# Kernel tuning notes

Hardware: AMD Instinct MI355X
Metric: run time of the kernel (lower is better)

Reference implementation:

```python
import jax, jax.numpy as jnp
import numpy as np

B, N, C = 2, 2048, 1024
H = 16
HD = C // H  # 64


def setup_inputs() -> dict:
    key = jax.random.key(0)
    k1, k2, k3 = jax.random.split(key, 3)
    x = jax.random.normal(k1, (B, N, C), dtype=jnp.float32)
    w_qkv = jax.random.normal(k2, (C, 3 * C), dtype=jnp.float32) * (C ** -0.5)
    b_qkv = jnp.zeros((3 * C,), dtype=jnp.float32)
    w_out = jax.random.normal(k3, (C, C), dtype=jnp.float32) * (C ** -0.5)
    b_out = jnp.zeros((C,), dtype=jnp.float32)
    return {"x": x, "w_qkv": w_qkv, "b_qkv": b_qkv, "w_out": w_out, "b_out": b_out}


def reference(x, w_qkv, b_qkv, w_out, b_out):
    scale = HD ** -0.5
    # QKV projection: (B,N,3C) -> (B,N,3,H,HD) -> (B,3,H,N,HD)
    qkv = (jnp.einsum('bnc,cd->bnd', x, w_qkv) + b_qkv)
    qkv = qkv.reshape(B, N, 3, H, HD).transpose(0, 2, 3, 1, 4)
    q, k, v = qkv[:, 0], qkv[:, 1], qkv[:, 2]  # each (B,H,N,HD)
    # scaled dot-product attention with full NxN matrix (as in source)
    attn = jnp.einsum('bhnd,bhmd->bhnm', q, k) * scale
    attn = jax.nn.softmax(attn, axis=-1)
    out = jnp.einsum('bhnm,bhmd->bhnd', attn, v)  # (B,H,N,HD)
    out = out.transpose(0, 2, 1, 3).reshape(B, N, C)
    out = jnp.einsum('bnc,cd->bnd', out, w_out) + b_out
    return out
```

## Files before the change

### kernel.cpp

```cpp
#include <hip/hip_runtime.h>
#include <stdint.h>

using uint = unsigned int;
using ushort = unsigned short;

constexpr int Bb = 2;
constexpr int Ns = 2048;
constexpr int Cd = 1024;
constexpr int Hh = 16;
constexpr int HD = 64;
constexpr int BHND = Bb * Hh * Ns * HD;

constexpr float QSCL = 0.18033688f;

typedef __attribute__((ext_vector_type(8))) short short8;
typedef __attribute__((ext_vector_type(4))) float floatx4;

__device__ inline ushort f2bf(float f) {
  uint u = __float_as_uint(f);
  return (ushort)((u + 0x7fffu + ((u >> 16) & 1u)) >> 16);
}
__device__ inline ushort f2bfr(float f) {
  return (ushort)((__float_as_uint(f) + 0x8000u) >> 16);
}
__device__ inline uint cvt_pk_bf16(float lo, float hi) {
  uint r;
  asm("v_cvt_pk_bf16_f32 %0, %1, %2" : "=v"(r) : "v"(lo), "v"(hi));
  return r;
}
__device__ inline void gld_lds16(const ushort* g, ushort* l) {
  __builtin_amdgcn_global_load_lds(
      (const __attribute__((address_space(1))) uint*)g,
      (__attribute__((address_space(3))) uint*)l, 16, 0, 0);
}

__global__ __launch_bounds__(256) void cvt_f32_bf16(
    const float* __restrict__ in, ushort* __restrict__ outp) {
  const int i = blockIdx.x * 256 + threadIdx.x;
  const float4 v = ((const float4*)in)[i];
  ushort4 o;
  o.x = f2bf(v.x); o.y = f2bf(v.y); o.z = f2bf(v.z); o.w = f2bf(v.w);
  ((ushort4*)outp)[i] = o;
}

__global__ __launch_bounds__(256) void transpose_f32_bf16(
    const float* __restrict__ in, ushort* __restrict__ outp, int R, int Cc) {
  __shared__ alignas(16) ushort tile[32][33];
  const int c0 = blockIdx.x * 32, r0 = blockIdx.y * 32;
  const int tx = threadIdx.x & 31;
  const int ty = threadIdx.x >> 5;
#pragma unroll
  for (int i = 0; i < 4; ++i)
    tile[ty + 8 * i][tx] = f2bf(in[(size_t)(r0 + ty + 8 * i) * Cc + c0 + tx]);
  __syncthreads();
#pragma unroll
  for (int i = 0; i < 4; ++i)
    outp[(size_t)(c0 + ty + 8 * i) * R + r0 + tx] = tile[tx][ty + 8 * i];
}

__global__ __launch_bounds__(256) void gemm_qkv(
    const ushort* __restrict__ A, const ushort* __restrict__ Bt,
    const float* __restrict__ bias, ushort* __restrict__ outp,
    int M, int K, int Nn) {
  __shared__ alignas(16) ushort As[2][128 * 32];
  __shared__ alignas(16) ushort Bs[2][128 * 32];
  const int tid = threadIdx.x;
  const int wave = tid >> 6, lane = tid & 63;
  const int quad = lane >> 4, l16 = lane & 15;
  const int wr = wave >> 1, wc = wave & 1;
  const int m0 = blockIdx.x * 128, n0 = blockIdx.y * 128;

  const int lrow = lane >> 2;
  const int lgr = lane & 3;
  const ushort* pa = A + (size_t)(m0 + wave * 32 + lrow) * K + lgr * 8;
  const ushort* pb = Bt + (size_t)(n0 + wave * 32 + lrow) * K + lgr * 8;
  const int lofs = wave * 32 * 32;

  floatx4 acc[4][4];
#pragma unroll
  for (int i = 0; i < 4; ++i)
#pragma unroll
    for (int j = 0; j < 4; ++j) {
      acc[i][j][0] = 0.f; acc[i][j][1] = 0.f; acc[i][j][2] = 0.f; acc[i][j][3] = 0.f;
    }

  const int nkt = K >> 5;
  gld_lds16(pa, &As[0][lofs]);
  gld_lds16(pa + (size_t)16 * K, &As[0][lofs + 16 * 32]);
  gld_lds16(pb, &Bs[0][lofs]);
  gld_lds16(pb + (size_t)16 * K, &Bs[0][lofs + 16 * 32]);
  __syncthreads();

  int cur = 0;
  for (int kt = 0; kt < nkt; ++kt) {
    if (kt + 1 < nkt) {
      const ushort* qa = pa + (size_t)(kt + 1) * 32;
      const ushort* qb = pb + (size_t)(kt + 1) * 32;
      gld_lds16(qa, &As[cur ^ 1][lofs]);
      gld_lds16(qa + (size_t)16 * K, &As[cur ^ 1][lofs + 16 * 32]);
      gld_lds16(qb, &Bs[cur ^ 1][lofs]);
      gld_lds16(qb + (size_t)16 * K, &Bs[cur ^ 1][lofs + 16 * 32]);
    }
    short8 af[4], bfv[4];
#pragma unroll
    for (int mt = 0; mt < 4; ++mt)
      af[mt] = *(const short8*)&As[cur][(wr * 64 + mt * 16 + l16) * 32 + quad * 8];
#pragma unroll
    for (int nt = 0; nt < 4; ++nt)
      bfv[nt] = *(const short8*)&Bs[cur][(wc * 64 + nt * 16 + l16) * 32 + quad * 8];
#pragma unroll
    for (int mt = 0; mt < 4; ++mt)
#pragma unroll
      for (int nt = 0; nt < 4; ++nt)
        acc[mt][nt] = __builtin_amdgcn_mfma_f32_16x16x32_bf16(af[mt], bfv[nt],
                                                              acc[mt][nt], 0, 0, 0);
    __syncthreads();
    cur ^= 1;
  }

  ushort* qp = outp;
  ushort* kp = qp + BHND;
  ushort* vp = qp + 2 * BHND;
#pragma unroll
  for (int nt = 0; nt < 4; ++nt) {
    const int gn = n0 + wc * 64 + nt * 16 + l16;
    const float bv = bias[gn];
    const int which = gn >> 10, cc = gn & 1023;
    const int h = cc >> 6, d = cc & 63;
    const float sc = (which == 0) ? QSCL : 1.0f;
#pragma unroll
    for (int mt = 0; mt < 4; ++mt) {
#pragma unroll
      for (int r = 0; r < 4; ++r) {
        const int gm = m0 + wr * 64 + mt * 16 + quad * 4 + r;
        const int b = gm >> 11, n = gm & 2047;
        const ushort o = f2bfr((acc[mt][nt][r] + bv) * sc);
        const int bh = b * Hh + h;
        if (which == 0)
          qp[((size_t)bh * Ns + n) * HD + d] = o;
        else if (which == 1)
          kp[((size_t)bh * Ns + n) * HD + d] = o;
        else
          vp[((size_t)bh * HD + d) * Ns + n] = o;
      }
    }
  }
}

__global__ __launch_bounds__(256) void gemm_out(
    const ushort* __restrict__ A, const ushort* __restrict__ Bt,
    const float* __restrict__ bias, float* __restrict__ fout,
    int M, int K, int Nn) {
  constexpr int LDT = 40;
  __shared__ alignas(16) ushort As[128 * LDT];
  __shared__ alignas(16) ushort Bs[128 * LDT];
  const int tid = threadIdx.x;
  const int wave = tid >> 6, lane = tid & 63;
  const int quad = lane >> 4, l16 = lane & 15;
  const int wr = wave >> 1, wc = wave & 1;
  const int m0 = blockIdx.x * 128, n0 = blockIdx.y * 128;

  const int srow0 = tid >> 2;
  const int skc = (tid & 3) * 8;

  const ushort* pa = A + (size_t)(m0 + srow0) * K + skc;
  const ushort* pb = Bt + (size_t)(n0 + srow0) * K + skc;

  floatx4 acc[4][4];
#pragma unroll
  for (int i = 0; i < 4; ++i)
#pragma unroll
    for (int j = 0; j < 4; ++j) {
      acc[i][j][0] = 0.f; acc[i][j][1] = 0.f; acc[i][j][2] = 0.f; acc[i][j][3] = 0.f;
    }

  uint4 ra0 = *(const uint4*)(pa);
  uint4 ra1 = *(const uint4*)(pa + (size_t)64 * K);
  uint4 rb0 = *(const uint4*)(pb);
  uint4 rb1 = *(const uint4*)(pb + (size_t)64 * K);

  const int nkt = K >> 5;
  for (int kt = 0; kt < nkt; ++kt) {
    __syncthreads();
    *(uint4*)&As[srow0 * LDT + skc] = ra0;
    *(uint4*)&As[(srow0 + 64) * LDT + skc] = ra1;
    *(uint4*)&Bs[srow0 * LDT + skc] = rb0;
    *(uint4*)&Bs[(srow0 + 64) * LDT + skc] = rb1;
    __syncthreads();
    if (kt + 1 < nkt) {
      const ushort* qa = pa + (size_t)(kt + 1) * 32;
      const ushort* qb = pb + (size_t)(kt + 1) * 32;
      ra0 = *(const uint4*)(qa);
      ra1 = *(const uint4*)(qa + (size_t)64 * K);
      rb0 = *(const uint4*)(qb);
      rb1 = *(const uint4*)(qb + (size_t)64 * K);
    }
    short8 af[4], bfv[4];
#pragma unroll
    for (int mt = 0; mt < 4; ++mt)
      af[mt] = *(const short8*)&As[(wr * 64 + mt * 16 + l16) * LDT + quad * 8];
#pragma unroll
    for (int nt = 0; nt < 4; ++nt)
      bfv[nt] = *(const short8*)&Bs[(wc * 64 + nt * 16 + l16) * LDT + quad * 8];
#pragma unroll
    for (int mt = 0; mt < 4; ++mt)
#pragma unroll
      for (int nt = 0; nt < 4; ++nt)
        acc[mt][nt] = __builtin_amdgcn_mfma_f32_16x16x32_bf16(af[mt], bfv[nt],
                                                              acc[mt][nt], 0, 0, 0);
  }

#pragma unroll
  for (int nt = 0; nt < 4; ++nt) {
    const int gn = n0 + wc * 64 + nt * 16 + l16;
    const float bv = bias[gn];
#pragma unroll
    for (int mt = 0; mt < 4; ++mt)
#pragma unroll
      for (int r = 0; r < 4; ++r) {
        const int gm = m0 + wr * 64 + mt * 16 + quad * 4 + r;
        fout[(size_t)gm * Nn + gn] = acc[mt][nt][r] + bv;
      }
  }
}

__global__ __launch_bounds__(256, 2) void attn(
    const ushort* __restrict__ q, const ushort* __restrict__ k,
    const ushort* __restrict__ vT, ushort* __restrict__ aout) {
  constexpr int LDK = 72;
  __shared__ alignas(16) ushort Ks[64 * LDK];
  __shared__ alignas(16) ushort Vs[64 * LDK];
  const int tid = threadIdx.x;
  const int wave = tid >> 6, lane = tid & 63;
  const int quad = lane >> 4, l16 = lane & 15;
  const int bh = blockIdx.y;
  const int qw = blockIdx.x * 128 + wave * 32;

  const ushort* kb = k + (size_t)bh * Ns * HD;
  const ushort* vb = vT + (size_t)bh * HD * Ns;

  short8 aq[2][2];
#pragma unroll
  for (int nqi = 0; nqi < 2; ++nqi) {
    const ushort* qp = q + ((size_t)bh * Ns + qw + nqi * 16 + l16) * HD + quad * 8;
    aq[nqi][0] = *(const short8*)(qp);
    aq[nqi][1] = *(const short8*)(qp + 32);
  }

  floatx4 accO[4][2];
#pragma unroll
  for (int mt = 0; mt < 4; ++mt)
#pragma unroll
    for (int nqi = 0; nqi < 2; ++nqi) {
      accO[mt][nqi][0] = 0.f; accO[mt][nqi][1] = 0.f;
      accO[mt][nqi][2] = 0.f; accO[mt][nqi][3] = 0.f;
    }
  float lst[2] = {0.f, 0.f};
  const floatx4 fz = {0.f, 0.f, 0.f, 0.f};

  const int srow = tid >> 2;
  const int g0 = (tid & 3) * 2;
  const int cbA = (g0 >> 2) * 8 + ((g0 >> 1) & 1);
  const int g1 = g0 + 1;
  const int cbB = (g1 >> 2) * 8 + 4 + ((g1 >> 1) & 1);

  const ushort* kgp = kb + (size_t)srow * HD + g0 * 8;
  const ushort* vgp = vb + (size_t)srow * Ns + g0 * 8;
  ushort* ksw = &Ks[srow * LDK + g0 * 8];
  ushort* vswA = &Vs[srow * LDK + cbA * 4];
  ushort* vswB = &Vs[srow * LDK + cbB * 4];

  uint4 kg0 = *(const uint4*)(kgp);
  uint4 kg1 = *(const uint4*)(kgp + 8);
  uint4 vg0 = *(const uint4*)(vgp);
  uint4 vg1 = *(const uint4*)(vgp + 8);
  const ushort* kpre = kgp + 64 * HD;
  const ushort* vpre = vgp + 64;

  for (int kv0 = 0; kv0 < Ns; kv0 += 64) {
    __syncthreads();
    *(uint4*)ksw = kg0;
    *(uint4*)(ksw + 8) = kg1;
    *(uint2*)vswA = make_uint2(vg0.x, vg0.y);
    *(uint2*)(vswA + 8) = make_uint2(vg0.z, vg0.w);
    *(uint2*)vswB = make_uint2(vg1.x, vg1.y);
    *(uint2*)(vswB + 8) = make_uint2(vg1.z, vg1.w);
    __syncthreads();

    short8 ak[4][2], av[4][2];
#pragma unroll
    for (int t4 = 0; t4 < 4; ++t4) {
      const int ro = (t4 * 16 + l16) * LDK + quad * 8;
      ak[t4][0] = *(const short8*)&Ks[ro];
      ak[t4][1] = *(const short8*)&Ks[ro + 32];
      av[t4][0] = *(const short8*)&Vs[ro];
      av[t4][1] = *(const short8*)&Vs[ro + 32];
    }
    if (kv0 + 64 < Ns) {
      kg0 = *(const uint4*)(kpre);
      kg1 = *(const uint4*)(kpre + 8);
      vg0 = *(const uint4*)(vpre);
      vg1 = *(const uint4*)(vpre + 8);
      kpre += 64 * HD;
      vpre += 64;
    }

#pragma unroll
    for (int nqi = 0; nqi < 2; ++nqi) {
      floatx4 sacc[4];
      __builtin_amdgcn_s_setprio(1);
#pragma unroll
      for (int kvt = 0; kvt < 4; ++kvt)
        sacc[kvt] = __builtin_amdgcn_mfma_f32_16x16x32_bf16(
            ak[kvt][0], aq[nqi][0], fz, 0, 0, 0);
#pragma unroll
      for (int kvt = 0; kvt < 4; ++kvt)
        sacc[kvt] = __builtin_amdgcn_mfma_f32_16x16x32_bf16(
            ak[kvt][1], aq[nqi][1], sacc[kvt], 0, 0, 0);
      __builtin_amdgcn_s_setprio(0);

      uint pk[4][2];
      float ls = 0.f;
#pragma unroll
      for (int kvt = 0; kvt < 4; ++kvt) {
        const float p0 = __builtin_amdgcn_exp2f(sacc[kvt][0]);
        const float p1 = __builtin_amdgcn_exp2f(sacc[kvt][1]);
        const float p2 = __builtin_amdgcn_exp2f(sacc[kvt][2]);
        const float p3 = __builtin_amdgcn_exp2f(sacc[kvt][3]);
        ls += (p0 + p1) + (p2 + p3);
        pk[kvt][0] = cvt_pk_bf16(p0, p1);
        pk[kvt][1] = cvt_pk_bf16(p2, p3);
      }
      lst[nqi] += ls;

      __builtin_amdgcn_s_setprio(1);
#pragma unroll
      for (int ks = 0; ks < 2; ++ks) {
        union { uint u[4]; short8 s; } pf;
        pf.u[0] = pk[2 * ks][0]; pf.u[1] = pk[2 * ks][1];
        pf.u[2] = pk[2 * ks + 1][0]; pf.u[3] = pk[2 * ks + 1][1];
#pragma unroll
        for (int mt = 0; mt < 4; ++mt)
          accO[mt][nqi] = __builtin_amdgcn_mfma_f32_16x16x32_bf16(
              av[mt][ks], pf.s, accO[mt][nqi], 0, 0, 0);
      }
      __builtin_amdgcn_s_setprio(0);
    }
  }

  const int b = bh >> 4, h = bh & 15;
#pragma unroll
  for (int nqi = 0; nqi < 2; ++nqi) {
    float l = lst[nqi];
    l += __shfl_xor(l, 16, 64);
    l += __shfl_xor(l, 32, 64);
    const float inv = 1.f / l;
    const int n = qw + nqi * 16 + l16;
#pragma unroll
    for (int mt = 0; mt < 4; ++mt) {
      ushort4 o;
      o.x = f2bfr(accO[mt][nqi][0] * inv);
      o.y = f2bfr(accO[mt][nqi][1] * inv);
      o.z = f2bfr(accO[mt][nqi][2] * inv);
      o.w = f2bfr(accO[mt][nqi][3] * inv);
      *(ushort4*)&aout[((size_t)(b * Ns + n)) * Cd + h * HD + mt * 16 + quad * 4] = o;
    }
  }
}

extern "C" void kernel_launch(void* const* d_in, const int* in_sizes, int n_in,
                              void* d_out, int out_size, void* d_ws, size_t ws_size,
                              hipStream_t stream) {
  (void)in_sizes; (void)n_in; (void)out_size; (void)ws_size;
  const float* x = (const float*)d_in[0];
  const float* w_qkv = (const float*)d_in[1];
  const float* b_qkv = (const float*)d_in[2];
  const float* w_out = (const float*)d_in[3];
  const float* b_out = (const float*)d_in[4];

  ushort* xbf = (ushort*)d_ws;
  ushort* wqkvT = xbf + (size_t)BHND;
  ushort* woutT = wqkvT + 3072 * 1024;
  ushort* qkvbuf = woutT + 1024 * 1024;
  ushort* aout = qkvbuf + 3 * (size_t)BHND;

  cvt_f32_bf16<<<dim3(BHND / 1024), 256, 0, stream>>>(x, xbf);
  transpose_f32_bf16<<<dim3(96, 32), 256, 0, stream>>>(w_qkv, wqkvT, 1024, 3072);
  transpose_f32_bf16<<<dim3(32, 32), 256, 0, stream>>>(w_out, woutT, 1024, 1024);

  gemm_qkv<<<dim3(32, 24), 256, 0, stream>>>(xbf, wqkvT, b_qkv, qkvbuf,
                                             4096, 1024, 3072);
  attn<<<dim3(16, 32), 256, 0, stream>>>(qkvbuf, qkvbuf + BHND,
                                         qkvbuf + 2 * (size_t)BHND, aout);
  gemm_out<<<dim3(32, 8), 256, 0, stream>>>(aout, woutT, b_out, (float*)d_out,
                                            4096, 1024, 1024);
}
```

Baseline: 186.7 us.

## Merge prep kernels into one launch and double attention KV tile to 128

Fuses the x conversion and both weight transposes into a single prep kernel dispatched by block index, removing two kernel launches. In attention, each iteration now stages 128 keys/values in LDS instead of 64, halving the number of barrier pairs and issuing prefetches for a larger chunk. This costs more LDS and registers per block, which may reduce occupancy or increase spills.

New measurement: 188.9 us. About the same (+1.2%).

```diff
diff --git a/kernel.cpp b/kernel.cpp
--- a/kernel.cpp
+++ b/kernel.cpp
@@ -34,21 +34,31 @@
       (__attribute__((address_space(3))) uint*)l, 16, 0, 0);
 }
 
-__global__ __launch_bounds__(256) void cvt_f32_bf16(
-    const float* __restrict__ in, ushort* __restrict__ outp) {
-  const int i = blockIdx.x * 256 + threadIdx.x;
-  const float4 v = ((const float4*)in)[i];
-  ushort4 o;
-  o.x = f2bf(v.x); o.y = f2bf(v.y); o.z = f2bf(v.z); o.w = f2bf(v.w);
-  ((ushort4*)outp)[i] = o;
-}
-
-__global__ __launch_bounds__(256) void transpose_f32_bf16(
-    const float* __restrict__ in, ushort* __restrict__ outp, int R, int Cc) {
+__global__ __launch_bounds__(256) void prep(
+    const float* __restrict__ x, ushort* __restrict__ xbf,
+    const float* __restrict__ w_qkv, ushort* __restrict__ wqkvT,
+    const float* __restrict__ w_out, ushort* __restrict__ woutT) {
   __shared__ alignas(16) ushort tile[32][33];
-  const int c0 = blockIdx.x * 32, r0 = blockIdx.y * 32;
-  const int tx = threadIdx.x & 31;
-  const int ty = threadIdx.x >> 5;
+  const int bid = blockIdx.x;
+  const int tid = threadIdx.x;
+  if (bid < 4096) {
+    const int i = bid * 256 + tid;
+    const float4 v = ((const float4*)x)[i];
+    ushort4 o;
+    o.x = f2bf(v.x); o.y = f2bf(v.y); o.z = f2bf(v.z); o.w = f2bf(v.w);
+    ((ushort4*)xbf)[i] = o;
+    return;
+  }
+  const float* in;
+  ushort* outp;
+  int Cc, idx;
+  if (bid < 7168) { idx = bid - 4096; in = w_qkv; outp = wqkvT; Cc = 3072; }
+  else            { idx = bid - 7168; in = w_out; outp = woutT; Cc = 1024; }
+  const int R = 1024;
+  const int nbx = Cc >> 5;
+  const int bx = idx % nbx, by = idx / nbx;
+  const int c0 = bx * 32, r0 = by * 32;
+  const int tx = tid & 31, ty = tid >> 5;
 #pragma unroll
   for (int i = 0; i < 4; ++i)
     tile[ty + 8 * i][tx] = f2bf(in[(size_t)(r0 + ty + 8 * i) * Cc + c0 + tx]);
@@ -228,8 +238,9 @@
     const ushort* __restrict__ q, const ushort* __restrict__ k,
     const ushort* __restrict__ vT, ushort* __restrict__ aout) {
   constexpr int LDK = 72;
-  __shared__ alignas(16) ushort Ks[64 * LDK];
-  __shared__ alignas(16) ushort Vs[64 * LDK];
+  constexpr int LDV = 136;
+  __shared__ alignas(16) ushort Ks[128 * LDK];
+  __shared__ alignas(16) ushort Vs[64 * LDV];
   const int tid = threadIdx.x;
   const int wave = tid >> 6, lane = tid & 63;
   const int quad = lane >> 4, l16 = lane & 15;
@@ -259,92 +270,122 @@
   const floatx4 fz = {0.f, 0.f, 0.f, 0.f};
 
   const int srow = tid >> 2;
-  const int g0 = (tid & 3) * 2;
-  const int cbA = (g0 >> 2) * 8 + ((g0 >> 1) & 1);
-  const int g1 = g0 + 1;
-  const int cbB = (g1 >> 2) * 8 + 4 + ((g1 >> 1) & 1);
-
-  const ushort* kgp = kb + (size_t)srow * HD + g0 * 8;
-  const ushort* vgp = vb + (size_t)srow * Ns + g0 * 8;
-  ushort* ksw = &Ks[srow * LDK + g0 * 8];
-  ushort* vswA = &Vs[srow * LDK + cbA * 4];
-  ushort* vswB = &Vs[srow * LDK + cbB * 4];
-
-  uint4 kg0 = *(const uint4*)(kgp);
-  uint4 kg1 = *(const uint4*)(kgp + 8);
+  const int gk = (tid & 3) * 2;
+  const ushort* kgp0 = kb + (size_t)srow * HD + gk * 8;
+  const ushort* kgp1 = kb + (size_t)(srow + 64) * HD + gk * 8;
+  ushort* ksw0 = &Ks[srow * LDK + gk * 8];
+  ushort* ksw1 = &Ks[(srow + 64) * LDK + gk * 8];
+
+  const int G0 = (tid & 3) * 4;
+  const int sHalf = G0 >> 3;
+  const int gp0 = G0 & 7;
+  const int cb0 = (gp0 >> 2) * 8 + ((gp0 >> 1) & 1);
+  const int cb1 = ((gp0 + 1) >> 2) * 8 + 4 + (((gp0 + 1) >> 1) & 1);
+  const int cb2 = ((gp0 + 2) >> 2) * 8 + (((gp0 + 2) >> 1) & 1);
+  const int cb3 = ((gp0 + 3) >> 2) * 8 + 4 + (((gp0 + 3) >> 1) & 1);
+  ushort* vw0 = &Vs[srow * LDV + sHalf * 64 + cb0 * 4];
+  ushort* vw1 = &Vs[srow * LDV + sHalf * 64 + cb1 * 4];
+  ushort* vw2 = &Vs[srow * LDV + sHalf * 64 + cb2 * 4];
+  ushort* vw3 = &Vs[srow * LDV + sHalf * 64 + cb3 * 4];
+  const ushort* vgp = vb + (size_t)srow * Ns + G0 * 8;
+
+  uint4 kg0 = *(const uint4*)(kgp0);
+  uint4 kg1 = *(const uint4*)(kgp0 + 8);
+  uint4 kg2 = *(const uint4*)(kgp1);
+  uint4 kg3 = *(const uint4*)(kgp1 + 8);
   uint4 vg0 = *(const uint4*)(vgp);
   uint4 vg1 = *(const uint4*)(vgp + 8);
-  const ushort* kpre = kgp + 64 * HD;
-  const ushort* vpre = vgp + 64;
-
-  for (int kv0 = 0; kv0 < Ns; kv0 += 64) {
+  uint4 vg2 = *(const uint4*)(vgp + 16);
+  uint4 vg3 = *(const uint4*)(vgp + 24);
+  const ushort* kpre0 = kgp0 + 128 * HD;
+  const ushort* kpre1 = kgp1 + 128 * HD;
+  const ushort* vpre = vgp + 128;
+
+  for (int kv0 = 0; kv0 < Ns; kv0 += 128) {
     __syncthreads();
-    *(uint4*)ksw = kg0;
-    *(uint4*)(ksw + 8) = kg1;
-    *(uint2*)vswA = make_uint2(vg0.x, vg0.y);
-    *(uint2*)(vswA + 8) = make_uint2(vg0.z, vg0.w);
-    *(uint2*)vswB = make_uint2(vg1.x, vg1.y);
-    *(uint2*)(vswB + 8) = make_uint2(vg1.z, vg1.w);
+    *(uint4*)ksw0 = kg0;
+    *(uint4*)(ksw0 + 8) = kg1;
+    *(uint4*)ksw1 = kg2;
+    *(uint4*)(ksw1 + 8) = kg3;
+    *(uint2*)vw0 = make_uint2(vg0.x, vg0.y);
+    *(uint2*)(vw0 + 8) = make_uint2(vg0.z, vg0.w);
+    *(uint2*)vw1 = make_uint2(vg1.x, vg1.y);
+    *(uint2*)(vw1 + 8) = make_uint2(vg1.z, vg1.w);
+    *(uint2*)vw2 = make_uint2(vg2.x, vg2.y);
+    *(uint2*)(vw2 + 8) = make_uint2(vg2.z, vg2.w);
+    *(uint2*)vw3 = make_uint2(vg3.x, vg3.y);
+    *(uint2*)(vw3 + 8) = make_uint2(vg3.z, vg3.w);
     __syncthreads();
 
-    short8 ak[4][2], av[4][2];
-#pragma unroll
-    for (int t4 = 0; t4 < 4; ++t4) {
-      const int ro = (t4 * 16 + l16) * LDK + quad * 8;
-      ak[t4][0] = *(const short8*)&Ks[ro];
-      ak[t4][1] = *(const short8*)&Ks[ro + 32];
-      av[t4][0] = *(const short8*)&Vs[ro];
-      av[t4][1] = *(const short8*)&Vs[ro + 32];
-    }
-    if (kv0 + 64 < Ns) {
-      kg0 = *(const uint4*)(kpre);
-      kg1 = *(const uint4*)(kpre + 8);
-      vg0 = *(const uint4*)(vpre);
-      vg1 = *(const uint4*)(vpre + 8);
-      kpre += 64 * HD;
-      vpre += 64;
-    }
-
-#pragma unroll
-    for (int nqi = 0; nqi < 2; ++nqi) {
-      floatx4 sacc[4];
-      __builtin_amdgcn_s_setprio(1);
-#pragma unroll
-      for (int kvt = 0; kvt < 4; ++kvt)
-        sacc[kvt] = __builtin_amdgcn_mfma_f32_16x16x32_bf16(
-            ak[kvt][0], aq[nqi][0], fz, 0, 0, 0);
-#pragma unroll
-      for (int kvt = 0; kvt < 4; ++kvt)
-        sacc[kvt] = __builtin_amdgcn_mfma_f32_16x16x32_bf16(
-            ak[kvt][1], aq[nqi][1], sacc[kvt], 0, 0, 0);
-      __builtin_amdgcn_s_setprio(0);
-
-      uint pk[4][2];
-      float ls = 0.f;
-#pragma unroll
-      for (int kvt = 0; kvt < 4; ++kvt) {
-        const float p0 = __builtin_amdgcn_exp2f(sacc[kvt][0]);
-        const float p1 = __builtin_amdgcn_exp2f(sacc[kvt][1]);
-        const float p2 = __builtin_amdgcn_exp2f(sacc[kvt][2]);
-        const float p3 = __builtin_amdgcn_exp2f(sacc[kvt][3]);
-        ls += (p0 + p1) + (p2 + p3);
-        pk[kvt][0] = cvt_pk_bf16(p0, p1);
-        pk[kvt][1] = cvt_pk_bf16(p2, p3);
+    bool first = true;
+#pragma unroll
+    for (int st = 0; st < 2; ++st) {
+      short8 ak[4][2], av[4][2];
+#pragma unroll
+      for (int t4 = 0; t4 < 4; ++t4) {
+        const int rk = (st * 64 + t4 * 16 + l16) * LDK + quad * 8;
+        const int rv = (t4 * 16 + l16) * LDV + st * 64 + quad * 8;
+        ak[t4][0] = *(const short8*)&Ks[rk];
+        ak[t4][1] = *(const short8*)&Ks[rk + 32];
+        av[t4][0] = *(const short8*)&Vs[rv];
+        av[t4][1] = *(const short8*)&Vs[rv + 32];
       }
-      lst[nqi] += ls;
-
-      __builtin_amdgcn_s_setprio(1);
-#pragma unroll
-      for (int ks = 0; ks < 2; ++ks) {
-        union { uint u[4]; short8 s; } pf;
-        pf.u[0] = pk[2 * ks][0]; pf.u[1] = pk[2 * ks][1];
-        pf.u[2] = pk[2 * ks + 1][0]; pf.u[3] = pk[2 * ks + 1][1];
-#pragma unroll
-        for (int mt = 0; mt < 4; ++mt)
-          accO[mt][nqi] = __builtin_amdgcn_mfma_f32_16x16x32_bf16(
-              av[mt][ks], pf.s, accO[mt][nqi], 0, 0, 0);
+      if (first && kv0 + 128 < Ns) {
+        kg0 = *(const uint4*)(kpre0);
+        kg1 = *(const uint4*)(kpre0 + 8);
+        kg2 = *(const uint4*)(kpre1);
+        kg3 = *(const uint4*)(kpre1 + 8);
+        vg0 = *(const uint4*)(vpre);
+        vg1 = *(const uint4*)(vpre + 8);
+        vg2 = *(const uint4*)(vpre + 16);
+        vg3 = *(const uint4*)(vpre + 24);
+        kpre0 += 128 * HD;
+        kpre1 += 128 * HD;
+        vpre += 128;
       }
-      __builtin_amdgcn_s_setprio(0);
+      first = false;
+
+#pragma unroll
+      for (int nqi = 0; nqi < 2; ++nqi) {
+        floatx4 sacc[4];
+        __builtin_amdgcn_s_setprio(1);
+#pragma unroll
+        for (int kvt = 0; kvt < 4; ++kvt)
+          sacc[kvt] = __builtin_amdgcn_mfma_f32_16x16x32_bf16(
+              ak[kvt][0], aq[nqi][0], fz, 0, 0, 0);
+#pragma unroll
+        for (int kvt = 0; kvt < 4; ++kvt)
+          sacc[kvt] = __builtin_amdgcn_mfma_f32_16x16x32_bf16(
+              ak[kvt][1], aq[nqi][1], sacc[kvt], 0, 0, 0);
+        __builtin_amdgcn_s_setprio(0);
+
+        uint pk[4][2];
+        float ls = 0.f;
+#pragma unroll
+        for (int kvt = 0; kvt < 4; ++kvt) {
+          const float p0 = __builtin_amdgcn_exp2f(sacc[kvt][0]);
+          const float p1 = __builtin_amdgcn_exp2f(sacc[kvt][1]);
+          const float p2 = __builtin_amdgcn_exp2f(sacc[kvt][2]);
+          const float p3 = __builtin_amdgcn_exp2f(sacc[kvt][3]);
+          ls += (p0 + p1) + (p2 + p3);
+          pk[kvt][0] = cvt_pk_bf16(p0, p1);
+          pk[kvt][1] = cvt_pk_bf16(p2, p3);
+        }
+        lst[nqi] += ls;
+
+        __builtin_amdgcn_s_setprio(1);
+#pragma unroll
+        for (int ks = 0; ks < 2; ++ks) {
+          union { uint u[4]; short8 s; } pf;
+          pf.u[0] = pk[2 * ks][0]; pf.u[1] = pk[2 * ks][1];
+          pf.u[2] = pk[2 * ks + 1][0]; pf.u[3] = pk[2 * ks + 1][1];
+#pragma unroll
+          for (int mt = 0; mt < 4; ++mt)
+            accO[mt][nqi] = __builtin_amdgcn_mfma_f32_16x16x32_bf16(
+                av[mt][ks], pf.s, accO[mt][nqi], 0, 0, 0);
+        }
+        __builtin_amdgcn_s_setprio(0);
+      }
     }
   }
 
@@ -384,9 +425,7 @@
   ushort* qkvbuf = woutT + 1024 * 1024;
   ushort* aout = qkvbuf + 3 * (size_t)BHND;
 
-  cvt_f32_bf16<<<dim3(BHND / 1024), 256, 0, stream>>>(x, xbf);
-  transpose_f32_bf16<<<dim3(96, 32), 256, 0, stream>>>(w_qkv, wqkvT, 1024, 3072);
-  transpose_f32_bf16<<<dim3(32, 32), 256, 0, stream>>>(w_out, woutT, 1024, 1024);
+  prep<<<dim3(8192), 256, 0, stream>>>(x, xbf, w_qkv, wqkvT, w_out, woutT);
 
   gemm_qkv<<<dim3(32, 24), 256, 0, stream>>>(xbf, wqkvT, b_qkv, qkvbuf,
                                              4096, 1024, 3072);
```

## Double-buffer K/V tiles in attention and merge prep kernels into one launch

Applied to the files above, without the earlier changes.

The attention kernel now keeps two LDS buffers for K and V. The next tile's global loads are written into the alternate buffer after compute, which cuts the per-tile barriers from two to one. The three preprocessing kernels (x conversion and two weight transposes) are fused into a single launch that dispatches on block index, saving launch overhead. LDS usage doubles, which may reduce occupancy for the attention kernel.

New measurement: 183.5 us. No clear change (-1.7%).

```diff
diff --git a/kernel.cpp b/kernel.cpp
--- a/kernel.cpp
+++ b/kernel.cpp
@@ -34,21 +34,31 @@
       (__attribute__((address_space(3))) uint*)l, 16, 0, 0);
 }
 
-__global__ __launch_bounds__(256) void cvt_f32_bf16(
-    const float* __restrict__ in, ushort* __restrict__ outp) {
-  const int i = blockIdx.x * 256 + threadIdx.x;
-  const float4 v = ((const float4*)in)[i];
-  ushort4 o;
-  o.x = f2bf(v.x); o.y = f2bf(v.y); o.z = f2bf(v.z); o.w = f2bf(v.w);
-  ((ushort4*)outp)[i] = o;
-}
-
-__global__ __launch_bounds__(256) void transpose_f32_bf16(
-    const float* __restrict__ in, ushort* __restrict__ outp, int R, int Cc) {
+__global__ __launch_bounds__(256) void prep(
+    const float* __restrict__ x, ushort* __restrict__ xbf,
+    const float* __restrict__ w_qkv, ushort* __restrict__ wqkvT,
+    const float* __restrict__ w_out, ushort* __restrict__ woutT) {
   __shared__ alignas(16) ushort tile[32][33];
-  const int c0 = blockIdx.x * 32, r0 = blockIdx.y * 32;
-  const int tx = threadIdx.x & 31;
-  const int ty = threadIdx.x >> 5;
+  const int bid = blockIdx.x;
+  const int tid = threadIdx.x;
+  if (bid < 4096) {
+    const int i = bid * 256 + tid;
+    const float4 v = ((const float4*)x)[i];
+    ushort4 o;
+    o.x = f2bf(v.x); o.y = f2bf(v.y); o.z = f2bf(v.z); o.w = f2bf(v.w);
+    ((ushort4*)xbf)[i] = o;
+    return;
+  }
+  const float* in;
+  ushort* outp;
+  int Cc, idx;
+  if (bid < 7168) { idx = bid - 4096; in = w_qkv; outp = wqkvT; Cc = 3072; }
+  else            { idx = bid - 7168; in = w_out; outp = woutT; Cc = 1024; }
+  const int R = 1024;
+  const int nbx = Cc >> 5;
+  const int bx = idx % nbx, by = idx / nbx;
+  const int c0 = bx * 32, r0 = by * 32;
+  const int tx = tid & 31, ty = tid >> 5;
 #pragma unroll
   for (int i = 0; i < 4; ++i)
     tile[ty + 8 * i][tx] = f2bf(in[(size_t)(r0 + ty + 8 * i) * Cc + c0 + tx]);
@@ -228,8 +238,8 @@
     const ushort* __restrict__ q, const ushort* __restrict__ k,
     const ushort* __restrict__ vT, ushort* __restrict__ aout) {
   constexpr int LDK = 72;
-  __shared__ alignas(16) ushort Ks[64 * LDK];
-  __shared__ alignas(16) ushort Vs[64 * LDK];
+  __shared__ alignas(16) ushort Ks[2][64 * LDK];
+  __shared__ alignas(16) ushort Vs[2][64 * LDK];
   const int tid = threadIdx.x;
   const int wave = tid >> 6, lane = tid & 63;
   const int quad = lane >> 4, l16 = lane & 15;
@@ -266,9 +276,9 @@
 
   const ushort* kgp = kb + (size_t)srow * HD + g0 * 8;
   const ushort* vgp = vb + (size_t)srow * Ns + g0 * 8;
-  ushort* ksw = &Ks[srow * LDK + g0 * 8];
-  ushort* vswA = &Vs[srow * LDK + cbA * 4];
-  ushort* vswB = &Vs[srow * LDK + cbB * 4];
+  const int kofs = srow * LDK + g0 * 8;
+  const int vofsA = srow * LDK + cbA * 4;
+  const int vofsB = srow * LDK + cbB * 4;
 
   uint4 kg0 = *(const uint4*)(kgp);
   uint4 kg1 = *(const uint4*)(kgp + 8);
@@ -277,74 +287,88 @@
   const ushort* kpre = kgp + 64 * HD;
   const ushort* vpre = vgp + 64;
 
-  for (int kv0 = 0; kv0 < Ns; kv0 += 64) {
-    __syncthreads();
-    *(uint4*)ksw = kg0;
-    *(uint4*)(ksw + 8) = kg1;
-    *(uint2*)vswA = make_uint2(vg0.x, vg0.y);
-    *(uint2*)(vswA + 8) = make_uint2(vg0.z, vg0.w);
-    *(uint2*)vswB = make_uint2(vg1.x, vg1.y);
-    *(uint2*)(vswB + 8) = make_uint2(vg1.z, vg1.w);
-    __syncthreads();
-
-    short8 ak[4][2], av[4][2];
-#pragma unroll
-    for (int t4 = 0; t4 < 4; ++t4) {
-      const int ro = (t4 * 16 + l16) * LDK + quad * 8;
-      ak[t4][0] = *(const short8*)&Ks[ro];
-      ak[t4][1] = *(const short8*)&Ks[ro + 32];
-      av[t4][0] = *(const short8*)&Vs[ro];
-      av[t4][1] = *(const short8*)&Vs[ro + 32];
-    }
-    if (kv0 + 64 < Ns) {
-      kg0 = *(const uint4*)(kpre);
-      kg1 = *(const uint4*)(kpre + 8);
-      vg0 = *(const uint4*)(vpre);
-      vg1 = *(const uint4*)(vpre + 8);
-      kpre += 64 * HD;
-      vpre += 64;
-    }
-
-#pragma unroll
-    for (int nqi = 0; nqi < 2; ++nqi) {
-      floatx4 sacc[4];
-      __builtin_amdgcn_s_setprio(1);
-#pragma unroll
-      for (int kvt = 0; kvt < 4; ++kvt)
-        sacc[kvt] = __builtin_amdgcn_mfma_f32_16x16x32_bf16(
-            ak[kvt][0], aq[nqi][0], fz, 0, 0, 0);
-#pragma unroll
-      for (int kvt = 0; kvt < 4; ++kvt)
-        sacc[kvt] = __builtin_amdgcn_mfma_f32_16x16x32_bf16(
-            ak[kvt][1], aq[nqi][1], sacc[kvt], 0, 0, 0);
-      __builtin_amdgcn_s_setprio(0);
-
-      uint pk[4][2];
-      float ls = 0.f;
-#pragma unroll
-      for (int kvt = 0; kvt < 4; ++kvt) {
-        const float p0 = __builtin_amdgcn_exp2f(sacc[kvt][0]);
-        const float p1 = __builtin_amdgcn_exp2f(sacc[kvt][1]);
-        const float p2 = __builtin_amdgcn_exp2f(sacc[kvt][2]);
-        const float p3 = __builtin_amdgcn_exp2f(sacc[kvt][3]);
-        ls += (p0 + p1) + (p2 + p3);
-        pk[kvt][0] = cvt_pk_bf16(p0, p1);
-        pk[kvt][1] = cvt_pk_bf16(p2, p3);
-      }
-      lst[nqi] += ls;
-
-      __builtin_amdgcn_s_setprio(1);
-#pragma unroll
-      for (int ks = 0; ks < 2; ++ks) {
-        union { uint u[4]; short8 s; } pf;
-        pf.u[0] = pk[2 * ks][0]; pf.u[1] = pk[2 * ks][1];
-        pf.u[2] = pk[2 * ks + 1][0]; pf.u[3] = pk[2 * ks + 1][1];
-#pragma unroll
-        for (int mt = 0; mt < 4; ++mt)
-          accO[mt][nqi] = __builtin_amdgcn_mfma_f32_16x16x32_bf16(
-              av[mt][ks], pf.s, accO[mt][nqi], 0, 0, 0);
-      }
-      __builtin_amdgcn_s_setprio(0);
+  *(uint4*)&Ks[0][kofs] = kg0;
+  *(uint4*)&Ks[0][kofs + 8] = kg1;
+  *(uint2*)&Vs[0][vofsA] = make_uint2(vg0.x, vg0.y);
+  *(uint2*)&Vs[0][vofsA + 8] = make_uint2(vg0.z, vg0.w);
+  *(uint2*)&Vs[0][vofsB] = make_uint2(vg1.x, vg1.y);
+  *(uint2*)&Vs[0][vofsB + 8] = make_uint2(vg1.z, vg1.w);
+  __syncthreads();
+
+  for (int kv0 = 0; kv0 < Ns; kv0 += 128) {
+#pragma unroll
+    for (int half = 0; half < 2; ++half) {
+      const bool more = kv0 + 64 * (half + 1) < Ns;
+
+      short8 ak[4][2], av[4][2];
+#pragma unroll
+      for (int t4 = 0; t4 < 4; ++t4) {
+        const int ro = (t4 * 16 + l16) * LDK + quad * 8;
+        ak[t4][0] = *(const short8*)&Ks[half][ro];
+        ak[t4][1] = *(const short8*)&Ks[half][ro + 32];
+        av[t4][0] = *(const short8*)&Vs[half][ro];
+        av[t4][1] = *(const short8*)&Vs[half][ro + 32];
+      }
+      if (more) {
+        kg0 = *(const uint4*)(kpre);
+        kg1 = *(const uint4*)(kpre + 8);
+        vg0 = *(const uint4*)(vpre);
+        vg1 = *(const uint4*)(vpre + 8);
+        kpre += 64 * HD;
+        vpre += 64;
+      }
+
+#pragma unroll
+      for (int nqi = 0; nqi < 2; ++nqi) {
+        floatx4 sacc[4];
+        __builtin_amdgcn_s_setprio(1);
+#pragma unroll
+        for (int kvt = 0; kvt < 4; ++kvt)
+          sacc[kvt] = __builtin_amdgcn_mfma_f32_16x16x32_bf16(
+              ak[kvt][0], aq[nqi][0], fz, 0, 0, 0);
+#pragma unroll
+        for (int kvt = 0; kvt < 4; ++kvt)
+          sacc[kvt] = __builtin_amdgcn_mfma_f32_16x16x32_bf16(
+              ak[kvt][1], aq[nqi][1], sacc[kvt], 0, 0, 0);
+        __builtin_amdgcn_s_setprio(0);
+
+        uint pk[4][2];
+        float ls = 0.f;
+#pragma unroll
+        for (int kvt = 0; kvt < 4; ++kvt) {
+          const float p0 = __builtin_amdgcn_exp2f(sacc[kvt][0]);
+          const float p1 = __builtin_amdgcn_exp2f(sacc[kvt][1]);
+          const float p2 = __builtin_amdgcn_exp2f(sacc[kvt][2]);
+          const float p3 = __builtin_amdgcn_exp2f(sacc[kvt][3]);
+          ls += (p0 + p1) + (p2 + p3);
+          pk[kvt][0] = cvt_pk_bf16(p0, p1);
+          pk[kvt][1] = cvt_pk_bf16(p2, p3);
+        }
+        lst[nqi] += ls;
+
+        __builtin_amdgcn_s_setprio(1);
+#pragma unroll
+        for (int ks = 0; ks < 2; ++ks) {
+          union { uint u[4]; short8 s; } pf;
+          pf.u[0] = pk[2 * ks][0]; pf.u[1] = pk[2 * ks][1];
+          pf.u[2] = pk[2 * ks + 1][0]; pf.u[3] = pk[2 * ks + 1][1];
+#pragma unroll
+          for (int mt = 0; mt < 4; ++mt)
+            accO[mt][nqi] = __builtin_amdgcn_mfma_f32_16x16x32_bf16(
+                av[mt][ks], pf.s, accO[mt][nqi], 0, 0, 0);
+        }
+        __builtin_amdgcn_s_setprio(0);
+      }
+
+      if (more) {
+        *(uint4*)&Ks[half ^ 1][kofs] = kg0;
+        *(uint4*)&Ks[half ^ 1][kofs + 8] = kg1;
+        *(uint2*)&Vs[half ^ 1][vofsA] = make_uint2(vg0.x, vg0.y);
+        *(uint2*)&Vs[half ^ 1][vofsA + 8] = make_uint2(vg0.z, vg0.w);
+        *(uint2*)&Vs[half ^ 1][vofsB] = make_uint2(vg1.x, vg1.y);
+        *(uint2*)&Vs[half ^ 1][vofsB + 8] = make_uint2(vg1.z, vg1.w);
+      }
+      __syncthreads();
     }
   }
 
@@ -384,9 +408,7 @@
   ushort* qkvbuf = woutT + 1024 * 1024;
   ushort* aout = qkvbuf + 3 * (size_t)BHND;
 
-  cvt_f32_bf16<<<dim3(BHND / 1024), 256, 0, stream>>>(x, xbf);
-  transpose_f32_bf16<<<dim3(96, 32), 256, 0, stream>>>(w_qkv, wqkvT, 1024, 3072);
-  transpose_f32_bf16<<<dim3(32, 32), 256, 0, stream>>>(w_out, woutT, 1024, 1024);
+  prep<<<dim3(8192), 256, 0, stream>>>(x, xbf, w_qkv, wqkvT, w_out, woutT);
 
   gemm_qkv<<<dim3(32, 24), 256, 0, stream>>>(xbf, wqkvT, b_qkv, qkvbuf,
                                              4096, 1024, 3072);
```
